# Kernel tuning notes

Hardware: AMD Instinct MI355X
Metric: run time of the kernel (lower is better)

## Reference

```python
import jax, jax.numpy as jnp
import numpy as np

B, T, C, H = 2, 2048, 1024, 16
D = C // H
SCALE = 1.0 / np.sqrt(D).astype(np.float32)


def setup_inputs() -> dict:
    key = jax.random.key(0)
    kx, kq, kk, kv, ko = jax.random.split(key, 5)
    s = 1.0 / np.sqrt(C).astype(np.float32)
    return {
        "x": jax.random.normal(kx, (B, T, C), dtype=jnp.float32),
        "wq": jax.random.normal(kq, (C, C), dtype=jnp.float32) * s,
        "wk": jax.random.normal(kk, (C, C), dtype=jnp.float32) * s,
        "wv": jax.random.normal(kv, (C, C), dtype=jnp.float32) * s,
        "wo": jax.random.normal(ko, (C, C), dtype=jnp.float32) * s,
    }


def reference(x, wq, wk, wv, wo):
    # nn.Linear(y) = y @ W.T; weights stored [out, in]
    q = (x @ wq.T).reshape(B, T, H, D).transpose(0, 2, 1, 3)  # [B,H,T,D]
    k = (x @ wk.T).reshape(B, T, H, D).transpose(0, 2, 1, 3)
    v = (x @ wv.T).reshape(B, T, H, D).transpose(0, 2, 1, 3)
    scores = jnp.einsum("bhqd,bhkd->bhqk", q, k) * SCALE  # [B,H,T,T]
    causal = jnp.tril(jnp.ones((T, T), dtype=bool))
    scores = jnp.where(causal, scores, -jnp.inf)
    attn = jax.nn.softmax(scores, axis=-1)
    out = jnp.einsum("bhqk,bhkd->bhqd", attn, v)  # [B,H,T,D]
    out = out.transpose(0, 2, 1, 3).reshape(B, T, C)
    return out @ wo.T
```

## Files before the change

kernel.cpp:

```cpp
#include <hip/hip_runtime.h>
#include <hip/hip_bf16.h>

#define B_ 2
#define T_ 2048
#define C_ 1024
#define H_ 16
#define D_ 64
#define M_ (B_*T_)
#define SCALE_ 0.125f
#define LOG2E_ 1.44269504f
#define NEG_ (-1e30f)
#define MOFF_ 12.0f

typedef __bf16 bf16;
typedef __bf16 bf16x4 __attribute__((ext_vector_type(4)));
typedef __bf16 bf16x8 __attribute__((ext_vector_type(8)));
typedef float  f32x4  __attribute__((ext_vector_type(4)));

#define XB_ELEMS  ((size_t)M_*C_)
#define W_ELEMS   ((size_t)C_*C_)

__device__ __forceinline__ void glds16(const void* g, void* l) {
  __builtin_amdgcn_global_load_lds((const __attribute__((address_space(1))) void*)g,
                                   (__attribute__((address_space(3))) void*)l,
                                   16, 0, 0);
}

__global__ __launch_bounds__(256)
void cvt5(const float* __restrict__ x,  const float* __restrict__ wq,
          const float* __restrict__ wk, const float* __restrict__ wv,
          const float* __restrict__ wo, bf16* __restrict__ out,
          bf16* __restrict__ wodst) {
  int bid = blockIdx.x;
  const float* src; bf16* dst; size_t off;
  if (bid < 2048)      { src = x;  dst = out;                         off = (size_t)bid*2048; }
  else if (bid < 2560) { src = wq; dst = out + XB_ELEMS;              off = (size_t)(bid-2048)*2048; }
  else if (bid < 3072) { src = wk; dst = out + XB_ELEMS +   W_ELEMS;  off = (size_t)(bid-2560)*2048; }
  else if (bid < 3584) { src = wv; dst = out + XB_ELEMS + 2*W_ELEMS;  off = (size_t)(bid-3072)*2048; }
  else                 { src = wo; dst = wodst;                       off = (size_t)(bid-3584)*2048; }
  size_t i = off + (size_t)threadIdx.x * 8;
  f32x4 lo = *(const f32x4*)(src + i);
  f32x4 hi = *(const f32x4*)(src + i + 4);
  bf16x8 r;
  #pragma unroll
  for (int t = 0; t < 4; ++t) { r[t] = (bf16)lo[t]; r[t+4] = (bf16)hi[t]; }
  *(bf16x8*)(dst + i) = r;
}

template<int OUTMODE>
__global__ __launch_bounds__(256)
void gemm_nt(const bf16* __restrict__ Ab,
             const bf16* __restrict__ W0, const bf16* __restrict__ W1,
             const bf16* __restrict__ W2,
             void* __restrict__ O0v, void* __restrict__ O1v, void* __restrict__ O2v,
             int K) {
  __shared__ __align__(16) bf16 As[128*64];
  __shared__ __align__(16) bf16 Bs[128*64];

  const bf16* W = W0;
  void* Ov = O0v;
  bool vtrans = false;
  float oscale = 1.0f;
  if constexpr (OUTMODE == 0) {
    if (blockIdx.z == 0)      { oscale = SCALE_ * LOG2E_; }
    else if (blockIdx.z == 1) { W = W1; Ov = O1v; }
    else                      { W = W2; Ov = O2v; vtrans = true; }
  }

  const int m0 = blockIdx.y * 128, n0 = blockIdx.x * 128;
  const int tid = threadIdx.x, wid = tid >> 6, lane = tid & 63;
  const int wm = wid >> 1, wn = wid & 1;
  const int l15 = lane & 15, grp = lane >> 4;

  f32x4 acc[4][4] = {};

  const int lr8 = lane >> 3;
  const int lkswz = ((lane & 7) ^ lr8) * 8;
  const bf16* Ag = Ab + (size_t)(m0 + wid*8 + lr8) * K + lkswz;
  const bf16* Bg = W  + (size_t)(n0 + wid*8 + lr8) * K + lkswz;

  const int amRow = wm*64 + l15;
  const int bnRow = wn*64 + l15;
  const int swz = l15 & 7;

  for (int k0 = 0; k0 < K; k0 += 64) {
    __syncthreads();
    #pragma unroll
    for (int c = 0; c < 4; ++c) {
      glds16(Ag + (size_t)(c*32)*K + k0, As + (wid + c*4)*512);
      glds16(Bg + (size_t)(c*32)*K + k0, Bs + (wid + c*4)*512);
    }
    __syncthreads();

    #pragma unroll
    for (int ks = 0; ks < 2; ++ks) {
      const int aslot = ((ks*4 + grp) ^ swz) * 8;
      bf16x8 af[4], bfr[4];
      #pragma unroll
      for (int i = 0; i < 4; ++i) {
        af[i]  = *(const bf16x8*)(As + (amRow + i*16)*64 + aslot);
        bfr[i] = *(const bf16x8*)(Bs + (bnRow + i*16)*64 + aslot);
      }
      __builtin_amdgcn_s_setprio(1);
      #pragma unroll
      for (int i = 0; i < 4; ++i)
        #pragma unroll
        for (int j = 0; j < 4; ++j)
          acc[i][j] = __builtin_amdgcn_mfma_f32_16x16x32_bf16(af[i], bfr[j], acc[i][j], 0, 0, 0);
      __builtin_amdgcn_s_setprio(0);
    }
  }

  const int rBase = m0 + wm*64 + grp * 4;
  const int cBase = n0 + wn*64 + l15;
  #pragma unroll
  for (int fm = 0; fm < 4; ++fm) {
    #pragma unroll
    for (int fn = 0; fn < 4; ++fn) {
      #pragma unroll
      for (int j = 0; j < 4; ++j) {
        int m = rBase + fm*16 + j;
        int n = cBase + fn*16;
        if constexpr (OUTMODE == 0) {
          int b = m >> 11, t = m & 2047, h = n >> 6, d = n & 63;
          size_t idx = vtrans ? (((size_t)(b*H_ + h) * D_ + d) * T_ + t)
                              : (((size_t)(b*H_ + h) * T_ + t) * D_ + d);
          ((bf16*)Ov)[idx] = (bf16)(acc[fm][fn][j] * oscale);
        } else {
          ((float*)Ov)[(size_t)m * C_ + n] = acc[fm][fn][j];
        }
      }
    }
  }
}

__global__ __launch_bounds__(256)
void attn_fwd(const bf16* __restrict__ Q, const bf16* __restrict__ Km,
              const bf16* __restrict__ Vt, bf16* __restrict__ Oa) {
  __shared__ __align__(16) bf16 Kd[2][64*64];
  __shared__ __align__(16) bf16 Vd[2][64*64];
  __shared__ __align__(16) bf16 Ps[64*64];

  const int id = blockIdx.x;
  const int qt = 31 - (id >> 5);
  const int bh = id & 31;
  const int q0 = qt * 64;
  const int tid = threadIdx.x, wid = tid >> 6, lane = tid & 63;
  const int l15 = lane & 15;
  const int grp = lane >> 4;
  const int myrow4 = grp * 4;
  const int sw = l15 & 7;

  const bf16* Qb = Q  + (size_t)bh * T_ * D_;
  const bf16* Kb = Km + (size_t)bh * T_ * D_;
  const bf16* Vb = Vt + (size_t)bh * D_ * T_;

  const int ksr = tid >> 3, kskc = tid & 7;
  const int wsl = (kskc ^ (ksr & 7)) * 8;
  const int b = bh >> 4, h = bh & 15;

  const int qrow = q0 + wid*16 + l15;
  bf16x8 aq0 = *(const bf16x8*)(Qb + (size_t)qrow*64 +      grp*8);
  bf16x8 aq1 = *(const bf16x8*)(Qb + (size_t)qrow*64 + 32 + grp*8);

  f32x4 oacc[4] = {};
  float l_s = 0.f;

  bf16x8 kv_a = *(const bf16x8*)(Kb + (size_t)(ksr)*64      + kskc*8);
  bf16x8 kv_b = *(const bf16x8*)(Kb + (size_t)(ksr + 32)*64 + kskc*8);
  bf16x8 vt_a = *(const bf16x8*)(Vb + (size_t)(ksr     )*T_ + kskc*8);
  bf16x8 vt_b = *(const bf16x8*)(Vb + (size_t)(ksr + 32)*T_ + kskc*8);
  *(bf16x8*)(Kd[0] + ksr*64      + wsl) = kv_a;
  *(bf16x8*)(Kd[0] + (ksr+32)*64 + wsl) = kv_b;
  *(bf16x8*)(Vd[0] + ksr*64      + wsl) = vt_a;
  *(bf16x8*)(Vd[0] + (ksr+32)*64 + wsl) = vt_b;
  {
    const int kn = (qt > 0) ? 64 : 0;
    kv_a = *(const bf16x8*)(Kb + (size_t)(kn + ksr)*64      + kskc*8);
    kv_b = *(const bf16x8*)(Kb + (size_t)(kn + ksr + 32)*64 + kskc*8);
    vt_a = *(const bf16x8*)(Vb + (size_t)(ksr     )*T_ + kn + kskc*8);
    vt_b = *(const bf16x8*)(Vb + (size_t)(ksr + 32)*T_ + kn + kskc*8);
  }
  __syncthreads();

  const int prow = wid*16 + l15;

  for (int kt = 0; kt <= qt; ++kt) {
    const int kv0 = kt * 64;
    const int cur = kt & 1;
    const bf16* Kc = Kd[cur];
    const bf16* Vc = Vd[cur];

    f32x4 s[4];
    __builtin_amdgcn_s_setprio(1);
    #pragma unroll
    for (int n = 0; n < 4; ++n) {
      int row = n*16 + l15;
      bf16x8 bk0 = *(const bf16x8*)(Kc + row*64 + ((grp     ^ sw)*8));
      bf16x8 bk1 = *(const bf16x8*)(Kc + row*64 + (((grp|4) ^ sw)*8));
      f32x4 a = {};
      a = __builtin_amdgcn_mfma_f32_16x16x32_bf16(bk0, aq0, a, 0, 0, 0);
      a = __builtin_amdgcn_mfma_f32_16x16x32_bf16(bk1, aq1, a, 0, 0, 0);
      s[n] = a;
    }
    __builtin_amdgcn_s_setprio(0);

    bf16x8 bv0[4];
    #pragma unroll
    for (int n = 0; n < 4; ++n)
      bv0[n] = *(const bf16x8*)(Vc + (n*16 + l15)*64 + ((grp ^ sw)*8));

    if (kt == qt) {
      #pragma unroll
      for (int n = 0; n < 4; ++n)
        #pragma unroll
        for (int j = 0; j < 4; ++j) {
          int kvg = kv0 + n*16 + myrow4 + j;
          s[n][j] = (kvg <= qrow) ? s[n][j] : NEG_;
        }
    }

    float ps = 0.f;
    #pragma unroll
    for (int n = 0; n < 4; ++n) {
      bf16x4 pw;
      #pragma unroll
      for (int j = 0; j < 4; ++j) {
        float p = __builtin_amdgcn_exp2f(s[n][j] - MOFF_);
        ps += p;
        pw[j] = (bf16)p;
      }
      int sl = (2*n + (grp >> 1)) ^ sw;
      *(bf16x4*)(Ps + prow*64 + sl*8 + (grp & 1)*4) = pw;
    }
    l_s += ps;

    asm volatile("s_waitcnt lgkmcnt(0)" ::: "memory");
    __builtin_amdgcn_sched_barrier(0);

    bf16x8 pa0 = *(const bf16x8*)(Ps + prow*64 + ((grp     ^ sw)*8));
    bf16x8 pa1 = *(const bf16x8*)(Ps + prow*64 + (((grp|4) ^ sw)*8));
    __builtin_amdgcn_s_setprio(1);
    #pragma unroll
    for (int n = 0; n < 4; ++n) {
      bf16x8 bv1 = *(const bf16x8*)(Vc + (n*16 + l15)*64 + (((grp|4) ^ sw)*8));
      oacc[n] = __builtin_amdgcn_mfma_f32_16x16x32_bf16(pa0, bv0[n], oacc[n], 0, 0, 0);
      oacc[n] = __builtin_amdgcn_mfma_f32_16x16x32_bf16(pa1, bv1,    oacc[n], 0, 0, 0);
    }
    __builtin_amdgcn_s_setprio(0);

    if (kt < qt) {
      *(bf16x8*)(Kd[cur^1] + ksr*64      + wsl) = kv_a;
      *(bf16x8*)(Kd[cur^1] + (ksr+32)*64 + wsl) = kv_b;
      *(bf16x8*)(Vd[cur^1] + ksr*64      + wsl) = vt_a;
      *(bf16x8*)(Vd[cur^1] + (ksr+32)*64 + wsl) = vt_b;
      const int kn = (kt + 2 <= qt) ? (kv0 + 128) : (kv0 + 64);
      kv_a = *(const bf16x8*)(Kb + (size_t)(kn + ksr)*64      + kskc*8);
      kv_b = *(const bf16x8*)(Kb + (size_t)(kn + ksr + 32)*64 + kskc*8);
      vt_a = *(const bf16x8*)(Vb + (size_t)(ksr     )*T_ + kn + kskc*8);
      vt_b = *(const bf16x8*)(Vb + (size_t)(ksr + 32)*T_ + kn + kskc*8);
    }
    __syncthreads();
  }

  l_s += __shfl_xor(l_s, 16);
  l_s += __shfl_xor(l_s, 32);
  const int tg = q0 + wid*16 + myrow4;
  #pragma unroll
  for (int j = 0; j < 4; ++j) {
    float lj = __shfl(l_s, myrow4 + j);
    float inv = 1.f / lj;
    int trow = tg + j;
    #pragma unroll
    for (int n = 0; n < 4; ++n) {
      int ch = h*64 + n*16 + l15;
      Oa[((size_t)(b*T_ + trow)) * C_ + ch] = (bf16)(oacc[n][j] * inv);
    }
  }
}

extern "C" void kernel_launch(void* const* d_in, const int* in_sizes, int n_in,
                              void* d_out, int out_size, void* d_ws, size_t ws_size,
                              hipStream_t stream) {
  const float* x  = (const float*)d_in[0];
  const float* wq = (const float*)d_in[1];
  const float* wk = (const float*)d_in[2];
  const float* wv = (const float*)d_in[3];
  const float* wo = (const float*)d_in[4];

  bf16* q  = (bf16*)d_ws;
  bf16* k  = q  + XB_ELEMS;
  bf16* v  = k  + XB_ELEMS;

  bf16* cvtbuf = (bf16*)d_out;
  bf16* xb  = cvtbuf;
  bf16* wqb = cvtbuf + XB_ELEMS;
  bf16* wkb = wqb + W_ELEMS;
  bf16* wvb = wkb + W_ELEMS;
  bf16* wob_stage = wvb + W_ELEMS;

  const bool bigws = ws_size >= (4*XB_ELEMS + W_ELEMS) * sizeof(bf16);
  bf16* ao  = bigws ? (v + XB_ELEMS) : xb;
  bf16* wob = bigws ? (v + 2*XB_ELEMS) : wob_stage;

  dim3 blk(256);
  cvt5<<<dim3(4096), blk, 0, stream>>>(x, wq, wk, wv, wo, cvtbuf, wob);
  gemm_nt<0><<<dim3(C_/128, M_/128, 3), blk, 0, stream>>>(xb, wqb, wkb, wvb,
                                                          q, k, v, C_);
  attn_fwd<<<dim3(1024), blk, 0, stream>>>(q, k, v, ao);
  bf16* aoSrc = ao;
  if (!bigws) {
    hipMemcpyAsync(q, xb,        XB_ELEMS * sizeof(bf16), hipMemcpyDeviceToDevice, stream);
    hipMemcpyAsync(k, wob_stage, W_ELEMS  * sizeof(bf16), hipMemcpyDeviceToDevice, stream);
    aoSrc = q; wob = k;
  }
  gemm_nt<1><<<dim3(C_/128, M_/128, 1), blk, 0, stream>>>(aoSrc, wob, nullptr, nullptr,
                                                          d_out, nullptr, nullptr, C_);
}
```

Before: 104.0 us.

## Process two query tiles per 512-thread block sharing K/V staging

The attention kernel now runs 512-thread blocks covering 128 query rows, with two 4-wave subgroups each handling a 64-row query tile and sharing one double-buffered K/V tile in LDS. This halves K/V global loads per query row and the per-thread staging work. The block schedule also changes from strictly longest-first to interleaving short and long tiles. The trade-off is that the first subgroup idles on the last KV tile and waits at the shared barriers, and there are half as many blocks, which may hurt occupancy or load balance.

```diff
diff --git a/kernel.cpp b/kernel.cpp
--- a/kernel.cpp
+++ b/kernel.cpp
@@ -134,23 +134,28 @@
   }
 }
 
-__global__ __launch_bounds__(256)
+__global__ __launch_bounds__(512)
 void attn_fwd(const bf16* __restrict__ Q, const bf16* __restrict__ Km,
               const bf16* __restrict__ Vt, bf16* __restrict__ Oa) {
   __shared__ __align__(16) bf16 Kd[2][64*64];
   __shared__ __align__(16) bf16 Vd[2][64*64];
-  __shared__ __align__(16) bf16 Ps[64*64];
+  __shared__ __align__(16) bf16 Ps[2][64*64];
 
   const int id = blockIdx.x;
-  const int qt = 31 - (id >> 5);
+  const int qt = (id < 256) ? (15 - (id >> 5)) : ((id - 256) >> 5);
   const int bh = id & 31;
-  const int q0 = qt * 64;
   const int tid = threadIdx.x, wid = tid >> 6, lane = tid & 63;
+  const int ss = wid >> 2;
+  const int w4 = wid & 3;
   const int l15 = lane & 15;
   const int grp = lane >> 4;
   const int myrow4 = grp * 4;
   const int sw = l15 & 7;
 
+  const int q0 = qt*128 + ss*64;
+  const int ktmax = 2*qt + 1;
+  const int diag  = 2*qt + ss;
+
   const bf16* Qb = Q  + (size_t)bh * T_ * D_;
   const bf16* Kb = Km + (size_t)bh * T_ * D_;
   const bf16* Vb = Vt + (size_t)bh * D_ * T_;
@@ -159,113 +164,106 @@
   const int wsl = (kskc ^ (ksr & 7)) * 8;
   const int b = bh >> 4, h = bh & 15;
 
-  const int qrow = q0 + wid*16 + l15;
+  const int qrow = q0 + w4*16 + l15;
   bf16x8 aq0 = *(const bf16x8*)(Qb + (size_t)qrow*64 +      grp*8);
   bf16x8 aq1 = *(const bf16x8*)(Qb + (size_t)qrow*64 + 32 + grp*8);
 
   f32x4 oacc[4] = {};
   float l_s = 0.f;
 
-  bf16x8 kv_a = *(const bf16x8*)(Kb + (size_t)(ksr)*64      + kskc*8);
-  bf16x8 kv_b = *(const bf16x8*)(Kb + (size_t)(ksr + 32)*64 + kskc*8);
-  bf16x8 vt_a = *(const bf16x8*)(Vb + (size_t)(ksr     )*T_ + kskc*8);
-  bf16x8 vt_b = *(const bf16x8*)(Vb + (size_t)(ksr + 32)*T_ + kskc*8);
-  *(bf16x8*)(Kd[0] + ksr*64      + wsl) = kv_a;
-  *(bf16x8*)(Kd[0] + (ksr+32)*64 + wsl) = kv_b;
-  *(bf16x8*)(Vd[0] + ksr*64      + wsl) = vt_a;
-  *(bf16x8*)(Vd[0] + (ksr+32)*64 + wsl) = vt_b;
+  bf16x8 kv_a = *(const bf16x8*)(Kb + (size_t)ksr*64 + kskc*8);
+  bf16x8 vt_a = *(const bf16x8*)(Vb + (size_t)ksr*T_ + kskc*8);
+  *(bf16x8*)(Kd[0] + ksr*64 + wsl) = kv_a;
+  *(bf16x8*)(Vd[0] + ksr*64 + wsl) = vt_a;
   {
-    const int kn = (qt > 0) ? 64 : 0;
-    kv_a = *(const bf16x8*)(Kb + (size_t)(kn + ksr)*64      + kskc*8);
-    kv_b = *(const bf16x8*)(Kb + (size_t)(kn + ksr + 32)*64 + kskc*8);
-    vt_a = *(const bf16x8*)(Vb + (size_t)(ksr     )*T_ + kn + kskc*8);
-    vt_b = *(const bf16x8*)(Vb + (size_t)(ksr + 32)*T_ + kn + kskc*8);
+    const int kn = (ktmax > 0) ? 64 : 0;
+    kv_a = *(const bf16x8*)(Kb + (size_t)(kn + ksr)*64 + kskc*8);
+    vt_a = *(const bf16x8*)(Vb + (size_t)ksr*T_ + kn + kskc*8);
   }
   __syncthreads();
 
-  const int prow = wid*16 + l15;
-
-  for (int kt = 0; kt <= qt; ++kt) {
+  const int prow = w4*16 + l15;
+  bf16* Pss = Ps[ss];
+
+  for (int kt = 0; kt <= ktmax; ++kt) {
     const int kv0 = kt * 64;
     const int cur = kt & 1;
     const bf16* Kc = Kd[cur];
     const bf16* Vc = Vd[cur];
 
-    f32x4 s[4];
-    __builtin_amdgcn_s_setprio(1);
-    #pragma unroll
-    for (int n = 0; n < 4; ++n) {
-      int row = n*16 + l15;
-      bf16x8 bk0 = *(const bf16x8*)(Kc + row*64 + ((grp     ^ sw)*8));
-      bf16x8 bk1 = *(const bf16x8*)(Kc + row*64 + (((grp|4) ^ sw)*8));
-      f32x4 a = {};
-      a = __builtin_amdgcn_mfma_f32_16x16x32_bf16(bk0, aq0, a, 0, 0, 0);
-      a = __builtin_amdgcn_mfma_f32_16x16x32_bf16(bk1, aq1, a, 0, 0, 0);
-      s[n] = a;
-    }
-    __builtin_amdgcn_s_setprio(0);
-
-    bf16x8 bv0[4];
-    #pragma unroll
-    for (int n = 0; n < 4; ++n)
-      bv0[n] = *(const bf16x8*)(Vc + (n*16 + l15)*64 + ((grp ^ sw)*8));
-
-    if (kt == qt) {
+    if (kt <= diag) {
+      f32x4 s[4];
+      __builtin_amdgcn_s_setprio(1);
+      #pragma unroll
+      for (int n = 0; n < 4; ++n) {
+        int row = n*16 + l15;
+        bf16x8 bk0 = *(const bf16x8*)(Kc + row*64 + ((grp     ^ sw)*8));
+        bf16x8 bk1 = *(const bf16x8*)(Kc + row*64 + (((grp|4) ^ sw)*8));
+        f32x4 a = {};
+        a = __builtin_amdgcn_mfma_f32_16x16x32_bf16(bk0, aq0, a, 0, 0, 0);
+        a = __builtin_amdgcn_mfma_f32_16x16x32_bf16(bk1, aq1, a, 0, 0, 0);
+        s[n] = a;
+      }
+      __builtin_amdgcn_s_setprio(0);
+
+      bf16x8 bv0[4];
       #pragma unroll
       for (int n = 0; n < 4; ++n)
+        bv0[n] = *(const bf16x8*)(Vc + (n*16 + l15)*64 + ((grp ^ sw)*8));
+
+      if (kt == diag) {
+        #pragma unroll
+        for (int n = 0; n < 4; ++n)
+          #pragma unroll
+          for (int j = 0; j < 4; ++j) {
+            int kvg = kv0 + n*16 + myrow4 + j;
+            s[n][j] = (kvg <= qrow) ? s[n][j] : NEG_;
+          }
+      }
+
+      float ps = 0.f;
+      #pragma unroll
+      for (int n = 0; n < 4; ++n) {
+        bf16x4 pw;
         #pragma unroll
         for (int j = 0; j < 4; ++j) {
-          int kvg = kv0 + n*16 + myrow4 + j;
-          s[n][j] = (kvg <= qrow) ? s[n][j] : NEG_;
+          float p = __builtin_amdgcn_exp2f(s[n][j] - MOFF_);
+          ps += p;
+          pw[j] = (bf16)p;
         }
-    }
-
-    float ps = 0.f;
-    #pragma unroll
-    for (int n = 0; n < 4; ++n) {
-      bf16x4 pw;
-      #pragma unroll
-      for (int j = 0; j < 4; ++j) {
-        float p = __builtin_amdgcn_exp2f(s[n][j] - MOFF_);
-        ps += p;
-        pw[j] = (bf16)p;
-      }
-      int sl = (2*n + (grp >> 1)) ^ sw;
-      *(bf16x4*)(Ps + prow*64 + sl*8 + (grp & 1)*4) = pw;
-    }
-    l_s += ps;
-
-    asm volatile("s_waitcnt lgkmcnt(0)" ::: "memory");
-    __builtin_amdgcn_sched_barrier(0);
-
-    bf16x8 pa0 = *(const bf16x8*)(Ps + prow*64 + ((grp     ^ sw)*8));
-    bf16x8 pa1 = *(const bf16x8*)(Ps + prow*64 + (((grp|4) ^ sw)*8));
-    __builtin_amdgcn_s_setprio(1);
-    #pragma unroll
-    for (int n = 0; n < 4; ++n) {
-      bf16x8 bv1 = *(const bf16x8*)(Vc + (n*16 + l15)*64 + (((grp|4) ^ sw)*8));
-      oacc[n] = __builtin_amdgcn_mfma_f32_16x16x32_bf16(pa0, bv0[n], oacc[n], 0, 0, 0);
-      oacc[n] = __builtin_amdgcn_mfma_f32_16x16x32_bf16(pa1, bv1,    oacc[n], 0, 0, 0);
-    }
-    __builtin_amdgcn_s_setprio(0);
-
-    if (kt < qt) {
-      *(bf16x8*)(Kd[cur^1] + ksr*64      + wsl) = kv_a;
-      *(bf16x8*)(Kd[cur^1] + (ksr+32)*64 + wsl) = kv_b;
-      *(bf16x8*)(Vd[cur^1] + ksr*64      + wsl) = vt_a;
-      *(bf16x8*)(Vd[cur^1] + (ksr+32)*64 + wsl) = vt_b;
-      const int kn = (kt + 2 <= qt) ? (kv0 + 128) : (kv0 + 64);
-      kv_a = *(const bf16x8*)(Kb + (size_t)(kn + ksr)*64      + kskc*8);
-      kv_b = *(const bf16x8*)(Kb + (size_t)(kn + ksr + 32)*64 + kskc*8);
-      vt_a = *(const bf16x8*)(Vb + (size_t)(ksr     )*T_ + kn + kskc*8);
-      vt_b = *(const bf16x8*)(Vb + (size_t)(ksr + 32)*T_ + kn + kskc*8);
+        int sl = (2*n + (grp >> 1)) ^ sw;
+        *(bf16x4*)(Pss + prow*64 + sl*8 + (grp & 1)*4) = pw;
+      }
+      l_s += ps;
+
+      asm volatile("s_waitcnt lgkmcnt(0)" ::: "memory");
+      __builtin_amdgcn_sched_barrier(0);
+
+      bf16x8 pa0 = *(const bf16x8*)(Pss + prow*64 + ((grp     ^ sw)*8));
+      bf16x8 pa1 = *(const bf16x8*)(Pss + prow*64 + (((grp|4) ^ sw)*8));
+      __builtin_amdgcn_s_setprio(1);
+      #pragma unroll
+      for (int n = 0; n < 4; ++n) {
+        bf16x8 bv1 = *(const bf16x8*)(Vc + (n*16 + l15)*64 + (((grp|4) ^ sw)*8));
+        oacc[n] = __builtin_amdgcn_mfma_f32_16x16x32_bf16(pa0, bv0[n], oacc[n], 0, 0, 0);
+        oacc[n] = __builtin_amdgcn_mfma_f32_16x16x32_bf16(pa1, bv1,    oacc[n], 0, 0, 0);
+      }
+      __builtin_amdgcn_s_setprio(0);
+    }
+
+    if (kt < ktmax) {
+      *(bf16x8*)(Kd[cur^1] + ksr*64 + wsl) = kv_a;
+      *(bf16x8*)(Vd[cur^1] + ksr*64 + wsl) = vt_a;
+      const int kn = (kt + 2 <= ktmax) ? (kv0 + 128) : (kv0 + 64);
+      kv_a = *(const bf16x8*)(Kb + (size_t)(kn + ksr)*64 + kskc*8);
+      vt_a = *(const bf16x8*)(Vb + (size_t)ksr*T_ + kn + kskc*8);
     }
     __syncthreads();
   }
 
   l_s += __shfl_xor(l_s, 16);
   l_s += __shfl_xor(l_s, 32);
-  const int tg = q0 + wid*16 + myrow4;
+  const int tg = q0 + w4*16 + myrow4;
   #pragma unroll
   for (int j = 0; j < 4; ++j) {
     float lj = __shfl(l_s, myrow4 + j);
@@ -307,7 +305,7 @@
   cvt5<<<dim3(4096), blk, 0, stream>>>(x, wq, wk, wv, wo, cvtbuf, wob);
   gemm_nt<0><<<dim3(C_/128, M_/128, 3), blk, 0, stream>>>(xb, wqb, wkb, wvb,
                                                           q, k, v, C_);
-  attn_fwd<<<dim3(1024), blk, 0, stream>>>(q, k, v, ao);
+  attn_fwd<<<dim3(512), dim3(512), 0, stream>>>(q, k, v, ao);
   bf16* aoSrc = ao;
   if (!bigws) {
     hipMemcpyAsync(q, xb,        XB_ELEMS * sizeof(bf16), hipMemcpyDeviceToDevice, stream);
```

Result: faster. 101.2 us (-2.6%).
